# Kernel optimization log

Hardware: AMD Instinct MI355X
Metric: run time of the kernel (lower is better)

The kernel has to match this reference:

```python
import jax, jax.numpy as jnp
import numpy as np

EPS = 1e-5  # BatchNorm2d default eps


def _binarize_ste(x):
    """Forward: sign(x). Backward: hardtanh STE (grad 1 where |x|<=1, else 0)."""
    xc = jnp.clip(x, -1.0, 1.0)
    return xc + jax.lax.stop_gradient(jnp.sign(x) - xc)


def setup_inputs() -> dict:
    key = jax.random.key(0)
    k1, k2, k3, k4 = jax.random.split(key, 4)
    x = jax.random.normal(k1, (32, 256, 32, 32), dtype=jnp.float32)
    # BatchNorm affine params (affine=True)
    gamma = 1.0 + 0.1 * jax.random.normal(k2, (256,), dtype=jnp.float32)
    beta = 0.1 * jax.random.normal(k3, (256,), dtype=jnp.float32)
    # Conv weight, OIHW, bias=False
    W = 0.05 * jax.random.normal(k4, (256, 256, 3, 3), dtype=jnp.float32)
    return {"x": x, "gamma": gamma, "beta": beta, "W": W}


def reference(x, gamma, beta, W):
    # BatchNorm2d, training-mode batch statistics over (N, H, W) per channel
    mean = jnp.mean(x, axis=(0, 2, 3), keepdims=True)
    var = jnp.var(x, axis=(0, 2, 3), keepdims=True)
    xn = (x - mean) * jax.lax.rsqrt(var + EPS)
    xn = xn * gamma[None, :, None, None] + beta[None, :, None, None]
    # Conv2d_1w1a: binarize activations and weights (sign fwd / STE bwd), then conv
    a = _binarize_ste(xn)
    wb = _binarize_ste(W)
    out = jax.lax.conv_general_dilated(
        a, wb,
        window_strides=(1, 1),
        padding=((1, 1), (1, 1)),
        dimension_numbers=("NCHW", "OIHW", "NCHW"),
    )
    return out
```

## Files before the change

### kernel.cpp

```cpp
#include <hip/hip_runtime.h>
#include <hip/hip_bf16.h>


#define NIMG 32
#define C    256
#define K    256

typedef int v4i  __attribute__((ext_vector_type(4)));
typedef int v16i __attribute__((ext_vector_type(16)));

#define AHT_IMG 295936
#define AHT_KB  36992
#define AHT_ROW 1088

__global__ __launch_bounds__(256) void k_stats_part(
    const float* __restrict__ x, double2* __restrict__ partials) {
  int grp = blockIdx.x;
  int c = blockIdx.y;
  int tid = threadIdx.x;
  double s = 0.0, sq = 0.0;
  #pragma unroll
  for (int ni = 0; ni < 4; ++ni) {
    int n = grp * 4 + ni;
    const float* p = x + (size_t)n * (C * 1024) + (size_t)c * 1024;
    float4 v = ((const float4*)p)[tid];
    s += (double)v.x + (double)v.y + (double)v.z + (double)v.w;
    sq += (double)v.x * v.x + (double)v.y * v.y
        + (double)v.z * v.z + (double)v.w * v.w;
  }
  for (int o = 32; o > 0; o >>= 1) {
    s += __shfl_down(s, o);
    sq += __shfl_down(sq, o);
  }
  __shared__ double ls[4], lq[4];
  if ((tid & 63) == 0) { ls[tid >> 6] = s; lq[tid >> 6] = sq; }
  __syncthreads();
  if (tid == 0) {
    double2 r;
    r.x = ls[0] + ls[1] + ls[2] + ls[3];
    r.y = lq[0] + lq[1] + lq[2] + lq[3];
    partials[c * 8 + grp] = r;
  }
}


__global__ __launch_bounds__(256) void k_packw_i8_final(
    const float* __restrict__ W, const double2* __restrict__ partials,
    const float* __restrict__ gamma, const float* __restrict__ beta,
    char* __restrict__ wfrag, float* __restrict__ t_out,
    unsigned* __restrict__ flip_out) {
  int bk = blockIdx.x;
  int tid = threadIdx.x;
  if (bk == 256) {
    int c = tid;
    double S = 0.0, Q = 0.0;
    #pragma unroll
    for (int g = 0; g < 8; ++g) {
      double2 p = partials[c * 8 + g];
      S += p.x; Q += p.y;
    }
    const double N = 32768.0;
    double mean = S / N;
    double var = Q / N - mean * mean;
    double rs = 1.0 / sqrt(var + 1e-5);
    double g = (double)gamma[c];
    double b = (double)beta[c];
    float t;
    unsigned flip;
    if (g == 0.0) {
      t = (b > 0.0) ? -3.0e38f : 3.0e38f;
      flip = 0u;
    } else {
      t = (float)(mean - b / (rs * g));
      flip = (g < 0.0) ? 1u : 0u;
    }
    t_out[c] = t;
    flip_out[c] = flip;
    return;
  }
  int k = bk, c = tid;
  const float* src = W + ((size_t)k * 256 + c) * 9;
  char* dst = wfrag + (size_t)(c >> 4) * 4096 + k * 16 + (c & 15);
  #pragma unroll
  for (int t = 0; t < 9; ++t)
    dst[(size_t)t * 65536] = (src[t] > 0.0f) ? (char)1 : (char)-1;
}

__global__ __launch_bounds__(256) void k_packa_i8(
    const float* __restrict__ x, const float* __restrict__ thr,
    const unsigned* __restrict__ flip, char* __restrict__ aHT) {
  __shared__ float lf[32 * 257];
  __shared__ float lthr[256];
  __shared__ unsigned lfl[256];
  int y = blockIdx.x, n = blockIdx.y, tid = threadIdx.x;
  lthr[tid] = thr[tid];
  lfl[tid] = flip[tid];
  #pragma unroll
  for (int it = 0; it < 8; ++it) {
    int c = it * 32 + (tid >> 3), q = tid & 7;
    float4 v = *(const float4*)(x + (size_t)n * 262144 + (size_t)c * 1024
                                + y * 32 + q * 4);
    lf[(q * 4 + 0) * 257 + c] = v.x;
    lf[(q * 4 + 1) * 257 + c] = v.y;
    lf[(q * 4 + 2) * 257 + c] = v.z;
    lf[(q * 4 + 3) * 257 + c] = v.w;
  }
  __syncthreads();
  int xl = tid & 31, cb = tid >> 5;
  unsigned wds[8];
  #pragma unroll
  for (int g = 0; g < 8; ++g) {
    unsigned wv = 0;
    #pragma unroll
    for (int jj = 0; jj < 4; ++jj) {
      int c = cb * 32 + g * 4 + jj;
      float v = lf[xl * 257 + c];
      unsigned bit = ((v > lthr[c]) ? 1u : 0u) ^ lfl[c];
      unsigned byte = bit ? 0x01u : 0xFFu;
      wv |= byte << (8 * jj);
    }
    wds[g] = wv;
  }
  char* dst = aHT + ((size_t)n * 8 + cb) * AHT_KB
            + (size_t)(y + 1) * AHT_ROW + (size_t)(xl + 1) * 32;
  uint4 u0, u1;
  u0.x = wds[0]; u0.y = wds[1]; u0.z = wds[2]; u0.w = wds[3];
  u1.x = wds[4]; u1.y = wds[5]; u1.z = wds[6]; u1.w = wds[7];
  *(uint4*)dst = u0;
  *((uint4*)dst + 1) = u1;

  uint4 z; z.x = 0; z.y = 0; z.z = 0; z.w = 0;
  if (xl < 2) {
    char* hz = aHT + ((size_t)n * 8 + cb) * AHT_KB
             + (size_t)(y + 1) * AHT_ROW + (size_t)(xl * 33) * 32;
    *(uint4*)hz = z;
    *((uint4*)hz + 1) = z;
  }
  if (y == 0 || y == 31) {
    int row = (y == 0) ? 0 : 33;
    for (int idx = tid; idx < 272; idx += 256) {
      int kb = idx / 34, xx = idx % 34;
      char* hz = aHT + ((size_t)n * 8 + kb) * AHT_KB
               + (size_t)row * AHT_ROW + (size_t)xx * 32;
      *(uint4*)hz = z;
      *((uint4*)hz + 1) = z;
    }
  }
}

__global__ __launch_bounds__(512) void k_conv_mfma(
    const char* __restrict__ aHT, const char* __restrict__ wfrag,
    float* __restrict__ out) {
  __shared__ uint4 lb4[2048];
  char* lb = (char*)lb4;
  int tid = threadIdx.x;
  int lane = tid & 63, w = tid >> 6;
  int bx = blockIdx.x;
  int n = bx >> 3, ys = bx & 7;
  int mb = w >> 2, nh = w & 3;
  int yw = ys * 4 + mb * 2;
  int xl = lane & 31, hi = lane >> 5;

  const char* abT = aHT + (size_t)n * AHT_IMG + (size_t)(xl + 1) * 32 + hi * 16;
  const char* wsrcA = wfrag + tid * 16;
  unsigned ldsoA = (unsigned)(tid * 16);
  unsigned bofs = (unsigned)(hi * 4096 + (nh * 64 + xl) * 16);

  v16i a00 = {0}, a01 = {0}, a10 = {0}, a11 = {0};
  v4i cA00, cA01, cA10, cA11;
  v4i nA00, nA01, nA10, nA11;
  uint4 wt0, wt1;

  {
    const char* ab = abT + (size_t)yw * AHT_ROW - 32;
    cA00 = *(const v4i*)(ab);
    cA01 = *(const v4i*)(ab + AHT_ROW);
    cA10 = *(const v4i*)(ab + AHT_KB);
    cA11 = *(const v4i*)(ab + AHT_KB + AHT_ROW);
    uint4 s0 = *(const uint4*)(wsrcA);
    uint4 s1 = *(const uint4*)(wsrcA + 8192);
    *(uint4*)(lb + ldsoA) = s0;
    *(uint4*)(lb + 8192 + ldsoA) = s1;
  }
  __syncthreads();

  for (int p = 0; p < 36; ++p) {
    int buf = (p & 1) << 14;
    if (p < 35) {
      int pp = p + 1;
      int tt = pp >> 2;
      int kb0 = (pp & 3) * 2;
      int dy = tt / 3 - 1, dx = tt % 3 - 1;
      const char* ab = abT + (size_t)kb0 * AHT_KB
                     + (size_t)(yw + dy + 1) * AHT_ROW + dx * 32;
      nA00 = *(const v4i*)(ab);
      nA01 = *(const v4i*)(ab + AHT_ROW);
      nA10 = *(const v4i*)(ab + AHT_KB);
      nA11 = *(const v4i*)(ab + AHT_KB + AHT_ROW);
      const char* wsrc = wsrcA + (size_t)pp * 16384;
      wt0 = *(const uint4*)(wsrc);
      wt1 = *(const uint4*)(wsrc + 8192);
    }
    {
      const char* bp0 = lb + buf + bofs;
      v4i b0 = *(const v4i*)(bp0);
      v4i b1 = *(const v4i*)(bp0 + 512);
      a00 = __builtin_amdgcn_mfma_i32_32x32x32_i8(cA00, b0, a00, 0, 0, 0);
      a01 = __builtin_amdgcn_mfma_i32_32x32x32_i8(cA00, b1, a01, 0, 0, 0);
      a10 = __builtin_amdgcn_mfma_i32_32x32x32_i8(cA01, b0, a10, 0, 0, 0);
      a11 = __builtin_amdgcn_mfma_i32_32x32x32_i8(cA01, b1, a11, 0, 0, 0);
      const char* bp1 = lb + buf + 8192 + bofs;
      v4i b2 = *(const v4i*)(bp1);
      v4i b3 = *(const v4i*)(bp1 + 512);
      a00 = __builtin_amdgcn_mfma_i32_32x32x32_i8(cA10, b2, a00, 0, 0, 0);
      a01 = __builtin_amdgcn_mfma_i32_32x32x32_i8(cA10, b3, a01, 0, 0, 0);
      a10 = __builtin_amdgcn_mfma_i32_32x32x32_i8(cA11, b2, a10, 0, 0, 0);
      a11 = __builtin_amdgcn_mfma_i32_32x32x32_i8(cA11, b3, a11, 0, 0, 0);
    }
    if (p < 35) {
      cA00 = nA00; cA01 = nA01; cA10 = nA10; cA11 = nA11;
      int nbuf = 16384 - buf;
      *(uint4*)(lb + nbuf + ldsoA) = wt0;
      *(uint4*)(lb + nbuf + 8192 + ldsoA) = wt1;
      __syncthreads();
    }
  }

  size_t ob0 = (size_t)n * 262144 + (size_t)(nh * 64 + xl) * 1024
             + (size_t)yw * 32 + 4 * hi;
  #pragma unroll
  for (int r = 0; r < 2; ++r) {
    #pragma unroll
    for (int nb = 0; nb < 2; ++nb) {
      v16i av = (r == 0) ? (nb == 0 ? a00 : a01) : (nb == 0 ? a10 : a11);
      float* obp = out + ob0 + (size_t)nb * 32768 + r * 32;
      #pragma unroll
      for (int q = 0; q < 4; ++q) {
        float4 f;
        f.x = (float)av[q * 4 + 0];
        f.y = (float)av[q * 4 + 1];
        f.z = (float)av[q * 4 + 2];
        f.w = (float)av[q * 4 + 3];
        *(float4*)(obp + 8 * q) = f;
      }
    }
  }
}


__global__ __launch_bounds__(256) void k_packw_corr_final(
    const float* __restrict__ W, const double2* __restrict__ partials,
    const float* __restrict__ gamma, const float* __restrict__ beta,
    unsigned* __restrict__ wp, int* __restrict__ corr,
    unsigned* __restrict__ zp, float* __restrict__ t_out,
    unsigned* __restrict__ flip_out) {
  int bk = blockIdx.x;
  int tid = threadIdx.x;
  if (bk == 256) {
    int c = tid;
    double S = 0.0, Q = 0.0;
    #pragma unroll
    for (int g = 0; g < 8; ++g) {
      double2 p = partials[c * 8 + g];
      S += p.x; Q += p.y;
    }
    const double N = 32768.0;
    double mean = S / N;
    double var = Q / N - mean * mean;
    double rs = 1.0 / sqrt(var + 1e-5);
    double g = (double)gamma[c];
    double b = (double)beta[c];
    float t;
    unsigned flip;
    if (g == 0.0) {
      t = (b > 0.0) ? -3.0e38f : 3.0e38f;
      flip = 0u;
    } else {
      t = (float)(mean - b / (rs * g));
      flip = (g < 0.0) ? 1u : 0u;
    }
    t_out[c] = t;
    flip_out[c] = flip;
    return;
  }
  int k = bk;
  __shared__ unsigned lw[72];
  float w[9];
  const float* src = W + (size_t)k * 2304 + (size_t)tid * 9;
  #pragma unroll
  for (int t = 0; t < 9; ++t) w[t] = src[t];
  int lane = tid & 63, wv = tid >> 6;
  #pragma unroll
  for (int t = 0; t < 9; ++t) {
    unsigned long long m = __ballot(w[t] > 0.0f);
    if (lane == 0) {
      lw[t * 8 + 2 * wv] = (unsigned)m;
      lw[t * 8 + 2 * wv + 1] = (unsigned)(m >> 32);
    }
  }
  __syncthreads();
  if (tid < 72) wp[(size_t)k * 72 + tid] = lw[tid];
  if (tid >= 128 && tid < 144) {
    int cls = tid - 128;
    int sum = 0;
    #pragma unroll
    for (int t = 0; t < 9; ++t) {
      int dy = t / 3 - 1, dx = t % 3 - 1;
      bool inv = (((cls & 1) && dx == -1) || ((cls & 2) && dx == 1) ||
                  ((cls & 4) && dy == -1) || ((cls & 8) && dy == 1));
      if (inv) {
        #pragma unroll
        for (int j = 0; j < 8; ++j) sum += __popc(lw[t * 8 + j]);
      }
    }
    corr[k * 16 + cls] = sum;
  }
  if (bk == 0 && tid >= 192 && tid < 200) zp[tid - 192] = 0u;
}

__global__ __launch_bounds__(256) void k_packa_bits(
    const float* __restrict__ x, const float* __restrict__ t,
    const unsigned* __restrict__ flip, unsigned* __restrict__ ap) {
  int n = blockIdx.y;
  int p0 = blockIdx.x * 64;
  int pix = threadIdx.x & 63;
  int q = threadIdx.x >> 6;
  unsigned w0 = 0, w1 = 0;
  const float* xb = x + (size_t)n * (C * 1024) + p0 + pix;
  #pragma unroll
  for (int i = 0; i < 64; ++i) {
    int c = q * 64 + i;
    float tv = t[c];
    unsigned fl = flip[c];
    float v = xb[(size_t)c * 1024];
    unsigned bit = ((v > tv) ? 1u : 0u) ^ fl;
    if (i < 32) w0 |= bit << i;
    else        w1 |= bit << (i - 32);
  }
  uint2 st; st.x = w0; st.y = w1;
  *(uint2*)(ap + ((size_t)n * 1024 + p0 + pix) * 8 + q * 2) = st;
}

__global__ __launch_bounds__(256) void k_conv_pop(
    const unsigned* __restrict__ ap, const unsigned* __restrict__ wp,
    const int* __restrict__ corr, const unsigned* __restrict__ zp,
    float* __restrict__ out) {
  int n = blockIdx.z;
  int ystrip = blockIdx.y;
  int kc = blockIdx.x;
  int tid = threadIdx.x;
  int lane = tid & 63;
  int wave = tid >> 6;
  int y = ystrip * 8 + wave * 2 + (lane >> 5);
  int xx = lane & 31;
  int cls = (xx == 0 ? 1 : 0) | (xx == 31 ? 2 : 0) |
            (y == 0 ? 4 : 0) | (y == 31 ? 8 : 0);
  uint4 a0[9], a1[9];
  int nv = 0;
  const uint4* zp4 = (const uint4*)zp;
  #pragma unroll
  for (int t = 0; t < 9; ++t) {
    int dy = t / 3 - 1, dx = t % 3 - 1;
    int cy = y + dy, cx = xx + dx;
    bool valid = (cy >= 0) & (cy < 32) & (cx >= 0) & (cx < 32);
    nv += valid ? 1 : 0;
    const uint4* pa = valid
        ? (const uint4*)(ap + (((size_t)n * 32 + cy) * 32 + cx) * 8)
        : zp4;
    a0[t] = pa[0];
    a1[t] = pa[1];
  }
  int bias = nv << 8;
  float* ob = out + (size_t)n * (K * 1024) + (size_t)y * 32 + xx;
  for (int kk = 0; kk < 16; ++kk) {
    int k = kc * 16 + kk;
    const uint4* wq = (const uint4*)(wp + (size_t)k * 72);
    int s0 = 0, s1 = 0, s2 = 0, s3 = 0, s4 = 0, s5 = 0, s6 = 0, s7 = 0;
    #pragma unroll
    for (int t = 0; t < 9; ++t) {
      uint4 wa = wq[t * 2];
      uint4 wb = wq[t * 2 + 1];
      s0 += __popc(a0[t].x ^ wa.x);
      s1 += __popc(a0[t].y ^ wa.y);
      s2 += __popc(a0[t].z ^ wa.z);
      s3 += __popc(a0[t].w ^ wa.w);
      s4 += __popc(a1[t].x ^ wb.x);
      s5 += __popc(a1[t].y ^ wb.y);
      s6 += __popc(a1[t].z ^ wb.z);
      s7 += __popc(a1[t].w ^ wb.w);
    }
    int S = ((s0 + s1) + (s2 + s3)) + ((s4 + s5) + (s6 + s7));
    int tot = corr[(k << 4) + cls] - S;
    ob[(size_t)k * 1024] = (float)(bias + 2 * tot);
  }
}


extern "C" void kernel_launch(void* const* d_in, const int* in_sizes, int n_in,
                              void* d_out, int out_size, void* d_ws, size_t ws_size,
                              hipStream_t stream) {
  const float* x = (const float*)d_in[0];
  const float* gamma = (const float*)d_in[1];
  const float* beta = (const float*)d_in[2];
  const float* W = (const float*)d_in[3];
  float* out = (float*)d_out;
  char* ws = (char*)d_ws;

  const size_t NEED = 655360 + (size_t)NIMG * AHT_IMG;
  if (ws_size >= NEED) {
    float* t = (float*)ws;
    unsigned* flip = (unsigned*)(ws + 1024);
    double2* partials = (double2*)(ws + 4096);
    char* wfrag = ws + 36864;
    char* aHT = ws + 655360;

    k_stats_part<<<dim3(8, 256), 256, 0, stream>>>(x, partials);
    k_packw_i8_final<<<257, 256, 0, stream>>>(W, partials, gamma, beta,
                                              wfrag, t, flip);
    k_packa_i8<<<dim3(32, 32), 256, 0, stream>>>(x, t, flip, aHT);
    k_conv_mfma<<<256, 512, 0, stream>>>(aHT, wfrag, out);
  } else {
    float* t = (float*)ws;
    unsigned* flip = (unsigned*)(ws + 1024);
    unsigned* wp = (unsigned*)(ws + 4096);
    unsigned* zp = (unsigned*)(ws + 77824);
    int* corr = (int*)(ws + 78336);
    double2* partials = (double2*)(ws + 98304);
    unsigned* ap = (unsigned*)(ws + 131072);

    k_stats_part<<<dim3(8, 256), 256, 0, stream>>>(x, partials);
    k_packw_corr_final<<<257, 256, 0, stream>>>(W, partials, gamma, beta,
                                                wp, corr, zp, t, flip);
    k_packa_bits<<<dim3(16, 32), 256, 0, stream>>>(x, t, flip, ap);
    k_conv_pop<<<dim3(16, 4, 32), 256, 0, stream>>>(ap, wp, corr, zp, out);
  }
}
```

Measured before the change: 57.35 us.

## Load conv weight fragments directly into registers, dropping LDS staging and barriers

The MFMA conv kernel no longer stages weight fragments through double-buffered shared memory with a per-iteration barrier. Each wave now loads its own B fragments from global memory into registers, prefetched one step ahead. Blocks shrink from 512 to 256 threads and the grid doubles, with a swizzled block index so neighbouring blocks share weights in cache. This removes LDS traffic and 35 barriers per block, but the weights are now fetched once per wave instead of once per block, so more traffic lands on L1/L2.

```diff
diff --git a/kernel.cpp b/kernel.cpp
--- a/kernel.cpp
+++ b/kernel.cpp
@@ -148,86 +148,70 @@
   }
 }
 
-__global__ __launch_bounds__(512) void k_conv_mfma(
+__global__ __launch_bounds__(256) void k_conv_mfma(
     const char* __restrict__ aHT, const char* __restrict__ wfrag,
     float* __restrict__ out) {
-  __shared__ uint4 lb4[2048];
-  char* lb = (char*)lb4;
   int tid = threadIdx.x;
-  int lane = tid & 63, w = tid >> 6;
+  int lane = tid & 63, nh = tid >> 6;
   int bx = blockIdx.x;
-  int n = bx >> 3, ys = bx & 7;
-  int mb = w >> 2, nh = w & 3;
-  int yw = ys * 4 + mb * 2;
+  int lb = (bx & 7) * 64 + (bx >> 3);
+  int n = lb >> 4, ys = lb & 15;
+  int y0 = ys * 2;
   int xl = lane & 31, hi = lane >> 5;
 
   const char* abT = aHT + (size_t)n * AHT_IMG + (size_t)(xl + 1) * 32 + hi * 16;
-  const char* wsrcA = wfrag + tid * 16;
-  unsigned ldsoA = (unsigned)(tid * 16);
-  unsigned bofs = (unsigned)(hi * 4096 + (nh * 64 + xl) * 16);
+  const char* wB = wfrag + hi * 4096 + (nh * 64 + xl) * 16;
 
   v16i a00 = {0}, a01 = {0}, a10 = {0}, a11 = {0};
-  v4i cA00, cA01, cA10, cA11;
-  v4i nA00, nA01, nA10, nA11;
-  uint4 wt0, wt1;
+  v4i cA00, cA01, cA10, cA11, nA00, nA01, nA10, nA11;
+  v4i cB0, cB1, cB2, cB3, nB0, nB1, nB2, nB3;
 
   {
-    const char* ab = abT + (size_t)yw * AHT_ROW - 32;
+    const char* ab = abT + (size_t)y0 * AHT_ROW - 32;
     cA00 = *(const v4i*)(ab);
     cA01 = *(const v4i*)(ab + AHT_ROW);
     cA10 = *(const v4i*)(ab + AHT_KB);
     cA11 = *(const v4i*)(ab + AHT_KB + AHT_ROW);
-    uint4 s0 = *(const uint4*)(wsrcA);
-    uint4 s1 = *(const uint4*)(wsrcA + 8192);
-    *(uint4*)(lb + ldsoA) = s0;
-    *(uint4*)(lb + 8192 + ldsoA) = s1;
-  }
-  __syncthreads();
+    cB0 = *(const v4i*)(wB);
+    cB1 = *(const v4i*)(wB + 512);
+    cB2 = *(const v4i*)(wB + 8192);
+    cB3 = *(const v4i*)(wB + 8192 + 512);
+  }
 
   for (int p = 0; p < 36; ++p) {
-    int buf = (p & 1) << 14;
     if (p < 35) {
       int pp = p + 1;
       int tt = pp >> 2;
       int kb0 = (pp & 3) * 2;
       int dy = tt / 3 - 1, dx = tt % 3 - 1;
       const char* ab = abT + (size_t)kb0 * AHT_KB
-                     + (size_t)(yw + dy + 1) * AHT_ROW + dx * 32;
+                     + (size_t)(y0 + dy + 1) * AHT_ROW + dx * 32;
       nA00 = *(const v4i*)(ab);
       nA01 = *(const v4i*)(ab + AHT_ROW);
       nA10 = *(const v4i*)(ab + AHT_KB);
       nA11 = *(const v4i*)(ab + AHT_KB + AHT_ROW);
-      const char* wsrc = wsrcA + (size_t)pp * 16384;
-      wt0 = *(const uint4*)(wsrc);
-      wt1 = *(const uint4*)(wsrc + 8192);
-    }
-    {
-      const char* bp0 = lb + buf + bofs;
-      v4i b0 = *(const v4i*)(bp0);
-      v4i b1 = *(const v4i*)(bp0 + 512);
-      a00 = __builtin_amdgcn_mfma_i32_32x32x32_i8(cA00, b0, a00, 0, 0, 0);
-      a01 = __builtin_amdgcn_mfma_i32_32x32x32_i8(cA00, b1, a01, 0, 0, 0);
-      a10 = __builtin_amdgcn_mfma_i32_32x32x32_i8(cA01, b0, a10, 0, 0, 0);
-      a11 = __builtin_amdgcn_mfma_i32_32x32x32_i8(cA01, b1, a11, 0, 0, 0);
-      const char* bp1 = lb + buf + 8192 + bofs;
-      v4i b2 = *(const v4i*)(bp1);
-      v4i b3 = *(const v4i*)(bp1 + 512);
-      a00 = __builtin_amdgcn_mfma_i32_32x32x32_i8(cA10, b2, a00, 0, 0, 0);
-      a01 = __builtin_amdgcn_mfma_i32_32x32x32_i8(cA10, b3, a01, 0, 0, 0);
-      a10 = __builtin_amdgcn_mfma_i32_32x32x32_i8(cA11, b2, a10, 0, 0, 0);
-      a11 = __builtin_amdgcn_mfma_i32_32x32x32_i8(cA11, b3, a11, 0, 0, 0);
-    }
+      const char* wp2 = wB + (size_t)pp * 16384;
+      nB0 = *(const v4i*)(wp2);
+      nB1 = *(const v4i*)(wp2 + 512);
+      nB2 = *(const v4i*)(wp2 + 8192);
+      nB3 = *(const v4i*)(wp2 + 8192 + 512);
+    }
+    a00 = __builtin_amdgcn_mfma_i32_32x32x32_i8(cA00, cB0, a00, 0, 0, 0);
+    a01 = __builtin_amdgcn_mfma_i32_32x32x32_i8(cA00, cB1, a01, 0, 0, 0);
+    a10 = __builtin_amdgcn_mfma_i32_32x32x32_i8(cA01, cB0, a10, 0, 0, 0);
+    a11 = __builtin_amdgcn_mfma_i32_32x32x32_i8(cA01, cB1, a11, 0, 0, 0);
+    a00 = __builtin_amdgcn_mfma_i32_32x32x32_i8(cA10, cB2, a00, 0, 0, 0);
+    a01 = __builtin_amdgcn_mfma_i32_32x32x32_i8(cA10, cB3, a01, 0, 0, 0);
+    a10 = __builtin_amdgcn_mfma_i32_32x32x32_i8(cA11, cB2, a10, 0, 0, 0);
+    a11 = __builtin_amdgcn_mfma_i32_32x32x32_i8(cA11, cB3, a11, 0, 0, 0);
     if (p < 35) {
       cA00 = nA00; cA01 = nA01; cA10 = nA10; cA11 = nA11;
-      int nbuf = 16384 - buf;
-      *(uint4*)(lb + nbuf + ldsoA) = wt0;
-      *(uint4*)(lb + nbuf + 8192 + ldsoA) = wt1;
-      __syncthreads();
+      cB0 = nB0; cB1 = nB1; cB2 = nB2; cB3 = nB3;
     }
   }
 
   size_t ob0 = (size_t)n * 262144 + (size_t)(nh * 64 + xl) * 1024
-             + (size_t)yw * 32 + 4 * hi;
+             + (size_t)y0 * 32 + 4 * hi;
   #pragma unroll
   for (int r = 0; r < 2; ++r) {
     #pragma unroll
@@ -418,7 +402,7 @@
     k_packw_i8_final<<<257, 256, 0, stream>>>(W, partials, gamma, beta,
                                               wfrag, t, flip);
     k_packa_i8<<<dim3(32, 32), 256, 0, stream>>>(x, t, flip, aHT);
-    k_conv_mfma<<<256, 512, 0, stream>>>(aHT, wfrag, out);
+    k_conv_mfma<<<512, 256, 0, stream>>>(aHT, wfrag, out);
   } else {
     float* t = (float*)ws;
     unsigned* flip = (unsigned*)(ws + 1024);
```

Result: faster. 50.51 us (-11.9%).
